# Performance work log

Hardware: AMD Instinct MI355X
Metric: run time of the kernel (lower is better)

The kernel has to match this reference:

```python
import jax, jax.numpy as jnp
import numpy as np

N, E, B = 50000, 800000, 512
IN, H, OUT = 128, 64, 32
BN_EPS = 1e-5


def setup_inputs() -> dict:
    key = jax.random.key(0)
    ks = jax.random.split(key, 32)
    inp = {}
    inp["x"] = jax.random.normal(ks[0], (N, IN), dtype=jnp.float32)
    inp["edge_index"] = jax.random.randint(ks[1], (2, E), 0, N, dtype=jnp.int64)
    inp["batch"] = jnp.sort(jax.random.randint(ks[2], (N,), 0, B, dtype=jnp.int64))
    inp["batch_size"] = B
    # GINConv MLP params: Linear(cin,H) -> BN(H) -> ReLU -> Linear(H,H)
    cins = [IN, H, H]
    ki = 3
    for i, cin in enumerate(cins):
        inp[f"c{i}_W1"] = jax.random.normal(ks[ki], (cin, H), dtype=jnp.float32) / np.sqrt(cin); ki += 1
        inp[f"c{i}_b1"] = jnp.zeros((H,), jnp.float32)
        inp[f"c{i}_g1"] = jnp.ones((H,), jnp.float32)
        inp[f"c{i}_bt1"] = jnp.zeros((H,), jnp.float32)
        inp[f"c{i}_W2"] = jax.random.normal(ks[ki], (H, H), dtype=jnp.float32) / np.sqrt(H); ki += 1
        inp[f"c{i}_b2"] = jnp.zeros((H,), jnp.float32)
    # final MLP (norm=None): Linear(H,H) -> ReLU -> [dropout, eval: identity] -> Linear(H,OUT)
    inp["f_W1"] = jax.random.normal(ks[ki], (H, H), dtype=jnp.float32) / np.sqrt(H); ki += 1
    inp["f_b1"] = jnp.zeros((H,), jnp.float32)
    inp["f_W2"] = jax.random.normal(ks[ki], (H, OUT), dtype=jnp.float32) / np.sqrt(H)
    inp["f_b2"] = jnp.zeros((OUT,), jnp.float32)
    return inp


def _bn(h, g, bt):
    # BatchNorm1d, training-mode statistics (biased variance), eps=1e-5
    mean = h.mean(axis=0)
    var = ((h - mean) ** 2).mean(axis=0)
    return g * (h - mean) * jax.lax.rsqrt(var + BN_EPS) + bt


def _gin_conv(x, src, dst, W1, b1, g1, bt1, W2, b2):
    # sum-aggregate neighbor features: agg[i] = sum_{(j->i)} x[j]
    agg = jax.ops.segment_sum(x[src], dst, num_segments=N)  # [N,H_in]
    h = x + agg  # (1+eps)*x + agg, eps=0
    h = jax.nn.relu(_bn(h @ W1 + b1, g1, bt1))
    return h @ W2 + b2


def reference(x, edge_index, batch, batch_size,
              c0_W1, c0_b1, c0_g1, c0_bt1, c0_W2, c0_b2,
              c1_W1, c1_b1, c1_g1, c1_bt1, c1_W2, c1_b2,
              c2_W1, c2_b1, c2_g1, c2_bt1, c2_W2, c2_b2,
              f_W1, f_b1, f_W2, f_b2):
    src, dst = edge_index[0], edge_index[1]
    convs = [(c0_W1, c0_b1, c0_g1, c0_bt1, c0_W2, c0_b2),
             (c1_W1, c1_b1, c1_g1, c1_bt1, c1_W2, c1_b2),
             (c2_W1, c2_b1, c2_g1, c2_bt1, c2_W2, c2_b2)]
    for p in convs:
        x = jax.nn.relu(_gin_conv(x, src, dst, *p))
    # global_add_pool over graph ids
    pooled = jax.ops.segment_sum(x, batch, num_segments=batch_size)  # [B,H]
    h = jax.nn.relu(pooled @ f_W1 + f_b1)  # dropout=0.5 skipped (eval mode)
    return h @ f_W2 + f_b2  # [B,OUT]
```

## Files before the change

kernel.cpp:

```cpp
#include <hip/hip_runtime.h>
#include <hip/hip_fp16.h>

#define NN 50000
#define EE 800000
#define BB 512
#define DIN 128
#define HH 64
#define DOUT 32
#define BN_EPS 1e-5f
#define SCAN_BLOCKS 196
#define GATHER_BLOCKS 2048
#define PADMAX (16 * NN + EE + 64)

template <int CIN>
__global__ __launch_bounds__(256) void proj_kernel(const float* __restrict__ X,
                                                   const float* __restrict__ W,
                                                   __half2* __restrict__ Qh)
{
    __shared__ float sW[CIN * 64];
    __shared__ float sX[16 * CIN];
    const int tid = threadIdx.x;
    const int row0 = blockIdx.x * 16;

    for (int i = tid; i < CIN * 16; i += 256)
        ((float4*)sW)[i] = ((const float4*)W)[i];
    const float* Xb = X + (size_t)row0 * CIN;
    for (int i = tid; i < 16 * CIN / 4; i += 256)
        ((float4*)sX)[i] = ((const float4*)Xb)[i];
    __syncthreads();

    const int col2 = tid & 31;
    const int rg   = tid >> 5;
    float2 acc0 = {0.f, 0.f};
    float2 acc1 = {0.f, 0.f};
    const float* x0p = &sX[(rg * 2 + 0) * CIN];
    const float* x1p = &sX[(rg * 2 + 1) * CIN];
#pragma unroll 4
    for (int k = 0; k < CIN; ++k) {
        const float2 w = *(const float2*)&sW[k * 64 + col2 * 2];
        const float x0 = x0p[k];
        const float x1 = x1p[k];
        acc0.x = fmaf(x0, w.x, acc0.x);
        acc0.y = fmaf(x0, w.y, acc0.y);
        acc1.x = fmaf(x1, w.x, acc1.x);
        acc1.y = fmaf(x1, w.y, acc1.y);
    }
    const int r0 = row0 + rg * 2;
    Qh[(size_t)(r0 + 0) * 32 + col2] = __floats2half2_rn(acc0.x, acc0.y);
    Qh[(size_t)(r0 + 1) * 32 + col2] = __floats2half2_rn(acc1.x, acc1.y);
}

__global__ __launch_bounds__(256) void fill_kernel(unsigned int* __restrict__ dstw)
{
    const int i = blockIdx.x * 256 + threadIdx.x;
    if (i < PADMAX / 2) dstw[i] = 0xC350C350u;
}

__global__ __launch_bounds__(256) void hist_rank_kernel(const int* __restrict__ dst,
                                                        int* __restrict__ deg,
                                                        unsigned short* __restrict__ rank)
{
    const int e = blockIdx.x * 256 + threadIdx.x;
    rank[e] = (unsigned short)atomicAdd(&deg[dst[e]], 1);
}

__global__ __launch_bounds__(256) void scanA_kernel(const int* __restrict__ deg,
                                                    int* __restrict__ poffs,
                                                    int* __restrict__ blockSums)
{
    __shared__ int s[256];
    const int t = threadIdx.x;
    const int i = blockIdx.x * 256 + t;
    int v = 0;
    if (i < NN) {
        const int d = deg[i];
        v = (d <= 16) ? 16 : ((d + 15) & ~15);
    }
    s[t] = v;
    __syncthreads();
    for (int off = 1; off < 256; off <<= 1) {
        const int a = (t >= off) ? s[t - off] : 0;
        __syncthreads();
        s[t] += a;
        __syncthreads();
    }
    if (i < NN) poffs[i] = s[t] - v;
    if (t == 255) blockSums[blockIdx.x] = s[255];
}

__global__ __launch_bounds__(256) void scanB_kernel(const int* __restrict__ blockSums,
                                                    int* __restrict__ blockOff,
                                                    int* __restrict__ poffs)
{
    __shared__ int s[256];
    const int t = threadIdx.x;
    const int v = (t < SCAN_BLOCKS) ? blockSums[t] : 0;
    s[t] = v;
    __syncthreads();
    for (int off = 1; off < 256; off <<= 1) {
        const int a = (t >= off) ? s[t - off] : 0;
        __syncthreads();
        s[t] += a;
        __syncthreads();
    }
    if (t < SCAN_BLOCKS) blockOff[t] = s[t] - v;
    if (t == SCAN_BLOCKS - 1) poffs[NN] = s[t];
}

__global__ __launch_bounds__(256) void scanC_kernel(int* __restrict__ poffs,
                                                    const int* __restrict__ blockOff,
                                                    float* __restrict__ statsbuf,
                                                    float* __restrict__ pooled,
                                                    unsigned int* __restrict__ qzero)
{
    const int i = blockIdx.x * 256 + threadIdx.x;
    if (i < NN) poffs[i] += blockOff[blockIdx.x];
    if (i < 384) statsbuf[i] = 0.f;
    if (i < BB * 64) pooled[i] = 0.f;
    if (blockIdx.x == 1 && threadIdx.x < 32) qzero[threadIdx.x] = 0u;
}

__global__ __launch_bounds__(256) void scatter_kernel(const int* __restrict__ src,
                                                      const int* __restrict__ dst,
                                                      const unsigned short* __restrict__ rank,
                                                      const int* __restrict__ poffs,
                                                      unsigned short* __restrict__ srcPadded)
{
    const int e = blockIdx.x * 256 + threadIdx.x;
    const int pos = poffs[dst[e]] + (int)rank[e];
    srcPadded[pos] = (unsigned short)src[e];
}

__global__ __launch_bounds__(256) void gather_kernel(const __half2* __restrict__ Qh,
                                                     const int* __restrict__ poffs,
                                                     const unsigned short* __restrict__ srcPadded,
                                                     const float* __restrict__ b1,
                                                     float* __restrict__ Z,
                                                     float* __restrict__ sums,
                                                     float* __restrict__ sumsq)
{
    const int tid   = threadIdx.x;
    const int lane  = tid & 63;
    const int wid   = tid >> 6;
    const int c     = lane & 31;
    const int grp   = lane >> 5;
    const int shamt = grp << 4;
    const uint* Qd  = (const uint*)Qh;
    const float2 bb = ((const float2*)b1)[c];

    float2 sa = {0.f, 0.f};
    float2 ta = {0.f, 0.f};

    for (int node = blockIdx.x * 4 + wid; node < NN; node += GATHER_BLOCKS * 4) {
        const int p0 = poffs[node];
        const int p1 = poffs[node + 1];
        const bool two = (p1 - p0) > 16;

        const uint4 ia = *(const uint4*)(srcPadded + p0);
        const uint4 ib = *(const uint4*)(srcPadded + p0 + 8);
        uint4 ia2, ib2;
        if (two) {
            ia2 = *(const uint4*)(srcPadded + p0 + 16);
            ib2 = *(const uint4*)(srcPadded + p0 + 24);
        }
        const uint sr = Qd[(size_t)node * 32 + c];

        uint r[16];
#pragma unroll
        for (int k = 0; k < 4; ++k) {
            r[k]     = Qd[(size_t)(((&ia.x)[k] >> shamt) & 0xffffu) * 32 + c];
            r[4 + k] = Qd[(size_t)(((&ib.x)[k] >> shamt) & 0xffffu) * 32 + c];
        }
        if (two) {
#pragma unroll
            for (int k = 0; k < 4; ++k) {
                r[8 + k]  = Qd[(size_t)(((&ia2.x)[k] >> shamt) & 0xffffu) * 32 + c];
                r[12 + k] = Qd[(size_t)(((&ib2.x)[k] >> shamt) & 0xffffu) * 32 + c];
            }
        }

        float2 acc = {0.f, 0.f};
#pragma unroll
        for (int k = 0; k < 8; ++k) {
            const float2 p = __half22float2(*(const __half2*)&r[k]);
            acc.x += p.x;
            acc.y += p.y;
        }
        if (two) {
#pragma unroll
            for (int k = 8; k < 16; ++k) {
                const float2 p = __half22float2(*(const __half2*)&r[k]);
                acc.x += p.x;
                acc.y += p.y;
            }
        }
        for (int j = p0 + 32; j < p1; j += 16) {
            const uint4 ja = *(const uint4*)(srcPadded + j);
            const uint4 jb = *(const uint4*)(srcPadded + j + 8);
            uint rr[8];
#pragma unroll
            for (int k = 0; k < 4; ++k) {
                rr[k]     = Qd[(size_t)(((&ja.x)[k] >> shamt) & 0xffffu) * 32 + c];
                rr[4 + k] = Qd[(size_t)(((&jb.x)[k] >> shamt) & 0xffffu) * 32 + c];
            }
#pragma unroll
            for (int k = 0; k < 8; ++k) {
                const float2 p = __half22float2(*(const __half2*)&rr[k]);
                acc.x += p.x;
                acc.y += p.y;
            }
        }

        acc.x += __shfl_xor(acc.x, 32);
        acc.y += __shfl_xor(acc.y, 32);

        if (grp == 0) {
            const float2 p = __half22float2(*(const __half2*)&sr);
            acc.x += p.x + bb.x;
            acc.y += p.y + bb.y;
            ((float2*)Z)[(size_t)node * 32 + c] = acc;
            sa.x += acc.x; sa.y += acc.y;
            ta.x += acc.x * acc.x; ta.y += acc.y * acc.y;
        }
    }

    __shared__ float red[4][32][4];
    if (grp == 0) {
        float* rp = red[wid][c];
        rp[0] = sa.x; rp[1] = sa.y; rp[2] = ta.x; rp[3] = ta.y;
    }
    __syncthreads();
    if (tid < 128) {
        const int c2 = tid >> 2;
        const int k  = tid & 3;
        const float v = red[0][c2][k] + red[1][c2][k] + red[2][c2][k] + red[3][c2][k];
        float* dstp;
        if (k == 0)      dstp = &sums[2 * c2 + 0];
        else if (k == 1) dstp = &sums[2 * c2 + 1];
        else if (k == 2) dstp = &sumsq[2 * c2 + 0];
        else             dstp = &sumsq[2 * c2 + 1];
        atomicAdd(dstp, v);
    }
}

template <bool POOL>
__global__ __launch_bounds__(256) void gemm2_kernel(const float* __restrict__ Z,
                                                    const float* __restrict__ sums,
                                                    const float* __restrict__ sumsq,
                                                    const float* __restrict__ g1,
                                                    const float* __restrict__ bt1,
                                                    const float* __restrict__ W2,
                                                    const float* __restrict__ b2,
                                                    const int* __restrict__ batch,
                                                    float* __restrict__ out)
{
    __shared__ float sW[64 * 64];
    __shared__ float sH[16 * 64];
    __shared__ float sScale[64];
    __shared__ float sShift[64];
    const int tid = threadIdx.x;
    const int row0 = blockIdx.x * 16;

    if (tid < 64) {
        const float inv_n = 1.0f / (float)NN;
        const float mean = sums[tid] * inv_n;
        const float var = fmaxf(sumsq[tid] * inv_n - mean * mean, 0.f);
        const float sc = g1[tid] * rsqrtf(var + BN_EPS);
        sScale[tid] = sc;
        sShift[tid] = bt1[tid] - mean * sc;
    }
    for (int i = tid; i < 64 * 16; i += 256)
        ((float4*)sW)[i] = ((const float4*)W2)[i];
    __syncthreads();

    const float4* Zb = (const float4*)(Z + (size_t)row0 * 64);
    {
        const int i = tid;
        const float4 z = Zb[i];
        const int c4 = i & 15;
        const float4 sc = ((const float4*)sScale)[c4];
        const float4 sh = ((const float4*)sShift)[c4];
        float4 h;
        h.x = fmaxf(fmaf(z.x, sc.x, sh.x), 0.f);
        h.y = fmaxf(fmaf(z.y, sc.y, sh.y), 0.f);
        h.z = fmaxf(fmaf(z.z, sc.z, sh.z), 0.f);
        h.w = fmaxf(fmaf(z.w, sc.w, sh.w), 0.f);
        ((float4*)sH)[i] = h;
    }
    __syncthreads();

    const int col = tid & 63;
    const int r0  = tid >> 6;
    const float bc = b2[col];
    float acc[4] = {bc, bc, bc, bc};
    for (int k = 0; k < 64; k += 4) {
        const float w0 = sW[(k + 0) * 64 + col];
        const float w1 = sW[(k + 1) * 64 + col];
        const float w2 = sW[(k + 2) * 64 + col];
        const float w3 = sW[(k + 3) * 64 + col];
#pragma unroll
        for (int rr = 0; rr < 4; ++rr) {
            const float4 hv = *(const float4*)&sH[(r0 + rr * 4) * 64 + k];
            acc[rr] = fmaf(hv.x, w0, acc[rr]);
            acc[rr] = fmaf(hv.y, w1, acc[rr]);
            acc[rr] = fmaf(hv.z, w2, acc[rr]);
            acc[rr] = fmaf(hv.w, w3, acc[rr]);
        }
    }
#pragma unroll
    for (int rr = 0; rr < 4; ++rr) {
        const int row = row0 + r0 + rr * 4;
        const float v = fmaxf(acc[rr], 0.f);
        if (POOL) {
            atomicAdd(&out[(size_t)batch[row] * 64 + col], v);
        } else {
            out[(size_t)row * 64 + col] = v;
        }
    }
}

__global__ __launch_bounds__(256) void final_mlp(const float* __restrict__ P,
                                                 const float* __restrict__ W1,
                                                 const float* __restrict__ b1,
                                                 const float* __restrict__ W2,
                                                 const float* __restrict__ b2,
                                                 float* __restrict__ out)
{
    __shared__ float sW1[64 * 64];
    __shared__ float sW2[64 * 32];
    __shared__ float sH[4 * 64];
    const int tid = threadIdx.x;
    const int row0 = blockIdx.x * 4;

    for (int i = tid; i < 1024; i += 256) ((float4*)sW1)[i] = ((const float4*)W1)[i];
    for (int i = tid; i < 512; i += 256) ((float4*)sW2)[i] = ((const float4*)W2)[i];
    __syncthreads();

    const int col = tid & 63;
    const int r = tid >> 6;
    float acc = b1[col];
    const float* prow = P + (size_t)(row0 + r) * 64;
    for (int k = 0; k < 64; ++k) acc = fmaf(prow[k], sW1[k * 64 + col], acc);
    sH[r * 64 + col] = fmaxf(acc, 0.f);
    __syncthreads();

    if (tid < 128) {
        const int c = tid & 31;
        const int r2 = tid >> 5;
        float a2 = b2[c];
        for (int k = 0; k < 64; ++k) a2 = fmaf(sH[r2 * 64 + k], sW2[k * 32 + c], a2);
        out[(size_t)(row0 + r2) * 32 + c] = a2;
    }
}

extern "C" void kernel_launch(void* const* d_in, const int* in_sizes, int n_in,
                              void* d_out, int out_size, void* d_ws, size_t ws_size,
                              hipStream_t stream)
{
    const float* x   = (const float*)d_in[0];
    const int* ei    = (const int*)d_in[1];
    const int* batch = (const int*)d_in[2];
    const float* cW1[3] = {(const float*)d_in[4],  (const float*)d_in[10], (const float*)d_in[16]};
    const float* cb1[3] = {(const float*)d_in[5],  (const float*)d_in[11], (const float*)d_in[17]};
    const float* cg1[3] = {(const float*)d_in[6],  (const float*)d_in[12], (const float*)d_in[18]};
    const float* cbt[3] = {(const float*)d_in[7],  (const float*)d_in[13], (const float*)d_in[19]};
    const float* cW2[3] = {(const float*)d_in[8],  (const float*)d_in[14], (const float*)d_in[20]};
    const float* cb2[3] = {(const float*)d_in[9],  (const float*)d_in[15], (const float*)d_in[21]};
    const float* fW1 = (const float*)d_in[22];
    const float* fb1 = (const float*)d_in[23];
    const float* fW2 = (const float*)d_in[24];
    const float* fb2 = (const float*)d_in[25];
    float* out = (float*)d_out;

    float* bufX     = (float*)d_ws;
    __half2* Qh     = (__half2*)(bufX + (size_t)NN * 64);
    float* pooled   = (float*)(Qh + (size_t)(NN + 1) * 32);
    float* statsbuf = pooled + (size_t)BB * 64;
    int* deg        = (int*)(statsbuf + 384);
    int* poffs      = deg + NN;
    int* blockSums  = poffs + (NN + 1);
    int* blockOff   = blockSums + 256;
    uintptr_t pa = ((uintptr_t)(blockOff + 256) + 15) & ~(uintptr_t)15;
    unsigned short* srcPadded = (unsigned short*)pa;
    unsigned short* rank      = srcPadded + PADMAX;

    const int* esrc = ei;
    const int* edst = ei + EE;

    const int gemm_blocks = NN / 16;
    const int edge_blocks = EE / 256;

    hipMemsetAsync(deg, 0, NN * sizeof(int), stream);
    fill_kernel<<<(PADMAX / 2 + 255) / 256, 256, 0, stream>>>((unsigned int*)srcPadded);
    hist_rank_kernel<<<edge_blocks, 256, 0, stream>>>(edst, deg, rank);
    scanA_kernel<<<SCAN_BLOCKS, 256, 0, stream>>>(deg, poffs, blockSums);
    scanB_kernel<<<1, 256, 0, stream>>>(blockSums, blockOff, poffs);
    scanC_kernel<<<SCAN_BLOCKS, 256, 0, stream>>>(poffs, blockOff, statsbuf, pooled,
                                                  (unsigned int*)(Qh + (size_t)NN * 32));
    scatter_kernel<<<edge_blocks, 256, 0, stream>>>(esrc, edst, rank, poffs, srcPadded);

    for (int layer = 0; layer < 3; ++layer) {
        float* sums  = statsbuf + layer * 128;
        float* sumsq = sums + 64;

        if (layer == 0)
            proj_kernel<DIN><<<gemm_blocks, 256, 0, stream>>>(x, cW1[0], Qh);
        else
            proj_kernel<HH><<<gemm_blocks, 256, 0, stream>>>(bufX, cW1[layer], Qh);

        gather_kernel<<<GATHER_BLOCKS, 256, 0, stream>>>(Qh, poffs, srcPadded, cb1[layer],
                                                         bufX, sums, sumsq);

        if (layer < 2) {
            gemm2_kernel<false><<<gemm_blocks, 256, 0, stream>>>(bufX, sums, sumsq, cg1[layer],
                                                                 cbt[layer], cW2[layer], cb2[layer],
                                                                 nullptr, bufX);
        } else {
            gemm2_kernel<true><<<gemm_blocks, 256, 0, stream>>>(bufX, sums, sumsq, cg1[layer],
                                                                cbt[layer], cW2[layer], cb2[layer],
                                                                batch, pooled);
        }
    }

    final_mlp<<<BB / 4, 256, 0, stream>>>(pooled, fW1, fb1, fW2, fb2, out);
}
```

Measured before the change: 365.1 us.

## Fuse second GEMM with next layer projection and prefetch next node in gather

For the first two layers, the W2 GEMM is fused with the next layer's W1 projection into one kernel. This removes a separate proj launch and the full fp32 write and re-read of the hidden activations. The gather loop now software-prefetches the next node's offsets, neighbor indices and self row while the current node's loads are in flight, to hide latency. The deg memset is folded into the fill kernel. Costs are more shared memory per block (two weight tiles plus an extra activation tile) and higher register pressure in the gather kernel.

```diff
diff --git a/kernel.cpp b/kernel.cpp
--- a/kernel.cpp
+++ b/kernel.cpp
@@ -50,10 +50,12 @@
     Qh[(size_t)(r0 + 1) * 32 + col2] = __floats2half2_rn(acc1.x, acc1.y);
 }
 
-__global__ __launch_bounds__(256) void fill_kernel(unsigned int* __restrict__ dstw)
+__global__ __launch_bounds__(256) void fill_kernel(unsigned int* __restrict__ dstw,
+                                                   int* __restrict__ deg)
 {
     const int i = blockIdx.x * 256 + threadIdx.x;
     if (i < PADMAX / 2) dstw[i] = 0xC350C350u;
+    if (i < NN) deg[i] = 0;
 }
 
 __global__ __launch_bounds__(256) void hist_rank_kernel(const int* __restrict__ dst,
@@ -150,21 +152,22 @@
 
     float2 sa = {0.f, 0.f};
     float2 ta = {0.f, 0.f};
-
-    for (int node = blockIdx.x * 4 + wid; node < NN; node += GATHER_BLOCKS * 4) {
-        const int p0 = poffs[node];
-        const int p1 = poffs[node + 1];
-        const bool two = (p1 - p0) > 16;
-
-        const uint4 ia = *(const uint4*)(srcPadded + p0);
-        const uint4 ib = *(const uint4*)(srcPadded + p0 + 8);
-        uint4 ia2, ib2;
-        if (two) {
-            ia2 = *(const uint4*)(srcPadded + p0 + 16);
-            ib2 = *(const uint4*)(srcPadded + p0 + 24);
-        }
-        const uint sr = Qd[(size_t)node * 32 + c];
-
+    const int step = GATHER_BLOCKS * 4;
+
+    int node = blockIdx.x * 4 + wid;
+    int p0 = poffs[node];
+    int p1 = poffs[node + 1];
+    uint4 ia = *(const uint4*)(srcPadded + p0);
+    uint4 ib = *(const uint4*)(srcPadded + p0 + 8);
+    bool two = (p1 - p0) > 16;
+    uint4 ia2 = {0, 0, 0, 0}, ib2 = {0, 0, 0, 0};
+    if (two) {
+        ia2 = *(const uint4*)(srcPadded + p0 + 16);
+        ib2 = *(const uint4*)(srcPadded + p0 + 24);
+    }
+    uint sr = Qd[(size_t)node * 32 + c];
+
+    while (true) {
         uint r[16];
 #pragma unroll
         for (int k = 0; k < 4; ++k) {
@@ -177,6 +180,26 @@
                 r[8 + k]  = Qd[(size_t)(((&ia2.x)[k] >> shamt) & 0xffffu) * 32 + c];
                 r[12 + k] = Qd[(size_t)(((&ib2.x)[k] >> shamt) & 0xffffu) * 32 + c];
             }
+        }
+
+        const int nnode = node + step;
+        const bool more = nnode < NN;
+        int np0 = 0, np1 = 0;
+        uint4 nia = {0, 0, 0, 0}, nib = {0, 0, 0, 0};
+        uint4 nia2 = {0, 0, 0, 0}, nib2 = {0, 0, 0, 0};
+        uint nsr = 0;
+        bool ntwo = false;
+        if (more) {
+            np0 = poffs[nnode];
+            np1 = poffs[nnode + 1];
+            nia = *(const uint4*)(srcPadded + np0);
+            nib = *(const uint4*)(srcPadded + np0 + 8);
+            ntwo = (np1 - np0) > 16;
+            if (ntwo) {
+                nia2 = *(const uint4*)(srcPadded + np0 + 16);
+                nib2 = *(const uint4*)(srcPadded + np0 + 24);
+            }
+            nsr = Qd[(size_t)nnode * 32 + c];
         }
 
         float2 acc = {0.f, 0.f};
@@ -222,6 +245,12 @@
             sa.x += acc.x; sa.y += acc.y;
             ta.x += acc.x * acc.x; ta.y += acc.y * acc.y;
         }
+
+        if (!more) break;
+        node = nnode; p0 = np0; p1 = np1;
+        ia = nia; ib = nib; two = ntwo;
+        if (two) { ia2 = nia2; ib2 = nib2; }
+        sr = nsr;
     }
 
     __shared__ float red[4][32][4];
@@ -243,19 +272,20 @@
     }
 }
 
-template <bool POOL>
-__global__ __launch_bounds__(256) void gemm2_kernel(const float* __restrict__ Z,
-                                                    const float* __restrict__ sums,
-                                                    const float* __restrict__ sumsq,
-                                                    const float* __restrict__ g1,
-                                                    const float* __restrict__ bt1,
-                                                    const float* __restrict__ W2,
-                                                    const float* __restrict__ b2,
-                                                    const int* __restrict__ batch,
-                                                    float* __restrict__ out)
-{
-    __shared__ float sW[64 * 64];
+__global__ __launch_bounds__(256) void gemm2proj_kernel(const float* __restrict__ Z,
+                                                        const float* __restrict__ sums,
+                                                        const float* __restrict__ sumsq,
+                                                        const float* __restrict__ g1,
+                                                        const float* __restrict__ bt1,
+                                                        const float* __restrict__ W2,
+                                                        const float* __restrict__ b2,
+                                                        const float* __restrict__ W1n,
+                                                        __half2* __restrict__ QhOut)
+{
+    __shared__ float sW2[64 * 64];
+    __shared__ float sW1[64 * 64];
     __shared__ float sH[16 * 64];
+    __shared__ float sA[16 * 64];
     __shared__ float sScale[64];
     __shared__ float sShift[64];
     const int tid = threadIdx.x;
@@ -269,8 +299,10 @@
         sScale[tid] = sc;
         sShift[tid] = bt1[tid] - mean * sc;
     }
-    for (int i = tid; i < 64 * 16; i += 256)
-        ((float4*)sW)[i] = ((const float4*)W2)[i];
+    for (int i = tid; i < 1024; i += 256) {
+        ((float4*)sW2)[i] = ((const float4*)W2)[i];
+        ((float4*)sW1)[i] = ((const float4*)W1n)[i];
+    }
     __syncthreads();
 
     const float4* Zb = (const float4*)(Z + (size_t)row0 * 64);
@@ -289,6 +321,99 @@
     }
     __syncthreads();
 
+    {
+        const int col = tid & 63;
+        const int r0  = tid >> 6;
+        const float bc = b2[col];
+        float acc[4] = {bc, bc, bc, bc};
+        for (int k = 0; k < 64; k += 4) {
+            const float w0 = sW2[(k + 0) * 64 + col];
+            const float w1 = sW2[(k + 1) * 64 + col];
+            const float w2 = sW2[(k + 2) * 64 + col];
+            const float w3 = sW2[(k + 3) * 64 + col];
+#pragma unroll
+            for (int rr = 0; rr < 4; ++rr) {
+                const float4 hv = *(const float4*)&sH[(r0 + rr * 4) * 64 + k];
+                acc[rr] = fmaf(hv.x, w0, acc[rr]);
+                acc[rr] = fmaf(hv.y, w1, acc[rr]);
+                acc[rr] = fmaf(hv.z, w2, acc[rr]);
+                acc[rr] = fmaf(hv.w, w3, acc[rr]);
+            }
+        }
+#pragma unroll
+        for (int rr = 0; rr < 4; ++rr)
+            sA[(r0 + rr * 4) * 64 + col] = fmaxf(acc[rr], 0.f);
+    }
+    __syncthreads();
+
+    {
+        const int col2 = tid & 31;
+        const int rg   = tid >> 5;
+        float2 acc0 = {0.f, 0.f};
+        float2 acc1 = {0.f, 0.f};
+        const float* a0p = &sA[(rg * 2 + 0) * 64];
+        const float* a1p = &sA[(rg * 2 + 1) * 64];
+#pragma unroll 4
+        for (int k = 0; k < 64; ++k) {
+            const float2 w = *(const float2*)&sW1[k * 64 + col2 * 2];
+            const float a0 = a0p[k];
+            const float a1 = a1p[k];
+            acc0.x = fmaf(a0, w.x, acc0.x);
+            acc0.y = fmaf(a0, w.y, acc0.y);
+            acc1.x = fmaf(a1, w.x, acc1.x);
+            acc1.y = fmaf(a1, w.y, acc1.y);
+        }
+        const int r0 = row0 + rg * 2;
+        QhOut[(size_t)(r0 + 0) * 32 + col2] = __floats2half2_rn(acc0.x, acc0.y);
+        QhOut[(size_t)(r0 + 1) * 32 + col2] = __floats2half2_rn(acc1.x, acc1.y);
+    }
+}
+
+__global__ __launch_bounds__(256) void gemm2pool_kernel(const float* __restrict__ Z,
+                                                        const float* __restrict__ sums,
+                                                        const float* __restrict__ sumsq,
+                                                        const float* __restrict__ g1,
+                                                        const float* __restrict__ bt1,
+                                                        const float* __restrict__ W2,
+                                                        const float* __restrict__ b2,
+                                                        const int* __restrict__ batch,
+                                                        float* __restrict__ out)
+{
+    __shared__ float sW[64 * 64];
+    __shared__ float sH[16 * 64];
+    __shared__ float sScale[64];
+    __shared__ float sShift[64];
+    const int tid = threadIdx.x;
+    const int row0 = blockIdx.x * 16;
+
+    if (tid < 64) {
+        const float inv_n = 1.0f / (float)NN;
+        const float mean = sums[tid] * inv_n;
+        const float var = fmaxf(sumsq[tid] * inv_n - mean * mean, 0.f);
+        const float sc = g1[tid] * rsqrtf(var + BN_EPS);
+        sScale[tid] = sc;
+        sShift[tid] = bt1[tid] - mean * sc;
+    }
+    for (int i = tid; i < 1024; i += 256)
+        ((float4*)sW)[i] = ((const float4*)W2)[i];
+    __syncthreads();
+
+    const float4* Zb = (const float4*)(Z + (size_t)row0 * 64);
+    {
+        const int i = tid;
+        const float4 z = Zb[i];
+        const int c4 = i & 15;
+        const float4 sc = ((const float4*)sScale)[c4];
+        const float4 sh = ((const float4*)sShift)[c4];
+        float4 h;
+        h.x = fmaxf(fmaf(z.x, sc.x, sh.x), 0.f);
+        h.y = fmaxf(fmaf(z.y, sc.y, sh.y), 0.f);
+        h.z = fmaxf(fmaf(z.z, sc.z, sh.z), 0.f);
+        h.w = fmaxf(fmaf(z.w, sc.w, sh.w), 0.f);
+        ((float4*)sH)[i] = h;
+    }
+    __syncthreads();
+
     const int col = tid & 63;
     const int r0  = tid >> 6;
     const float bc = b2[col];
@@ -311,11 +436,7 @@
     for (int rr = 0; rr < 4; ++rr) {
         const int row = row0 + r0 + rr * 4;
         const float v = fmaxf(acc[rr], 0.f);
-        if (POOL) {
-            atomicAdd(&out[(size_t)batch[row] * 64 + col], v);
-        } else {
-            out[(size_t)row * 64 + col] = v;
-        }
+        atomicAdd(&out[(size_t)batch[row] * 64 + col], v);
     }
 }
 
@@ -390,8 +511,7 @@
     const int gemm_blocks = NN / 16;
     const int edge_blocks = EE / 256;
 
-    hipMemsetAsync(deg, 0, NN * sizeof(int), stream);
-    fill_kernel<<<(PADMAX / 2 + 255) / 256, 256, 0, stream>>>((unsigned int*)srcPadded);
+    fill_kernel<<<(PADMAX / 2 + 255) / 256, 256, 0, stream>>>((unsigned int*)srcPadded, deg);
     hist_rank_kernel<<<edge_blocks, 256, 0, stream>>>(edst, deg, rank);
     scanA_kernel<<<SCAN_BLOCKS, 256, 0, stream>>>(deg, poffs, blockSums);
     scanB_kernel<<<1, 256, 0, stream>>>(blockSums, blockOff, poffs);
@@ -399,26 +519,23 @@
                                                   (unsigned int*)(Qh + (size_t)NN * 32));
     scatter_kernel<<<edge_blocks, 256, 0, stream>>>(esrc, edst, rank, poffs, srcPadded);
 
+    proj_kernel<DIN><<<gemm_blocks, 256, 0, stream>>>(x, cW1[0], Qh);
+
     for (int layer = 0; layer < 3; ++layer) {
         float* sums  = statsbuf + layer * 128;
         float* sumsq = sums + 64;
 
-        if (layer == 0)
-            proj_kernel<DIN><<<gemm_blocks, 256, 0, stream>>>(x, cW1[0], Qh);
-        else
-            proj_kernel<HH><<<gemm_blocks, 256, 0, stream>>>(bufX, cW1[layer], Qh);
-
         gather_kernel<<<GATHER_BLOCKS, 256, 0, stream>>>(Qh, poffs, srcPadded, cb1[layer],
                                                          bufX, sums, sumsq);
 
         if (layer < 2) {
-            gemm2_kernel<false><<<gemm_blocks, 256, 0, stream>>>(bufX, sums, sumsq, cg1[layer],
-                                                                 cbt[layer], cW2[layer], cb2[layer],
-                                                                 nullptr, bufX);
+            gemm2proj_kernel<<<gemm_blocks, 256, 0, stream>>>(bufX, sums, sumsq, cg1[layer],
+                                                              cbt[layer], cW2[layer], cb2[layer],
+                                                              cW1[layer + 1], Qh);
         } else {
-            gemm2_kernel<true><<<gemm_blocks, 256, 0, stream>>>(bufX, sums, sumsq, cg1[layer],
-                                                                cbt[layer], cW2[layer], cb2[layer],
-                                                                batch, pooled);
+            gemm2pool_kernel<<<gemm_blocks, 256, 0, stream>>>(bufX, sums, sumsq, cg1[layer],
+                                                              cbt[layer], cW2[layer], cb2[layer],
+                                                              batch, pooled);
         }
     }
 
```

Result: faster. 350.9 us (-3.9%).
